# Kernel optimization log

Hardware: AMD Instinct MI355X
Metric: run time of the kernel (lower is better)

## Reference

```python
import jax, jax.numpy as jnp
import numpy as np

B, N, D, H = 2048, 64, 256, 16

def setup_inputs() -> dict:
    key = jax.random.key(0)
    ks = jax.random.split(key, 6)
    members_embeds = jax.random.normal(ks[0], (B, N, D), dtype=jnp.float32)
    item_embeds = jax.random.normal(ks[1], (B, D), dtype=jnp.float32)
    # MLP params: Linear(D,16) -> ReLU -> Linear(16,1)
    W1 = jax.random.normal(ks[2], (D, H), dtype=jnp.float32) * (1.0 / np.sqrt(D))
    b1 = jnp.zeros((H,), dtype=jnp.float32)
    W2 = jax.random.normal(ks[3], (H, 1), dtype=jnp.float32) * (1.0 / np.sqrt(H))
    b2 = jnp.zeros((1,), dtype=jnp.float32)
    return {"members_embeds": members_embeds, "item_embeds": item_embeds,
            "W1": W1, "b1": b1, "W2": W2, "b2": b2}

def reference(members_embeds, item_embeds, W1, b1, W2, b2):
    # Original: diff_i = sum_{j != i} (u_i - u_j) * item  ==  (N*u_i - sum_j u_j) * item
    n = members_embeds.shape[1]
    total = jnp.sum(members_embeds, axis=1, keepdims=True)           # [B,1,D]
    diff = (n * members_embeds - total) * item_embeds[:, None, :]    # [B,N,D]
    h = jax.nn.relu(jnp.einsum('bnd,dh->bnh', diff, W1) + b1)        # [B,N,16]
    logits = (jnp.einsum('bnh,ho->bno', h, W2) + b2)[..., 0]         # [B,N]
    return jax.nn.softmax(logits, axis=1)                            # weights over members
```

## Files before the change

### kernel.cpp

```cpp
#include <hip/hip_runtime.h>


static constexpr int NMEM  = 64;
static constexpr int DDIM  = 256;
static constexpr int TD    = 32;
static constexpr int NTILE = DDIM / TD;
static constexpr int UTS4  = TD / 4;

__device__ __forceinline__ void fma4(float4& acc, float s, const float4& w) {
    acc.x = fmaf(s, w.x, acc.x);
    acc.y = fmaf(s, w.y, acc.y);
    acc.z = fmaf(s, w.z, acc.z);
    acc.w = fmaf(s, w.w, acc.w);
}

__global__ __launch_bounds__(256, 2)
void attn_group_softmax(const float* __restrict__ u_g,
                        const float* __restrict__ item_g,
                        const float* __restrict__ W1,
                        const float* __restrict__ b1,
                        const float* __restrict__ W2,
                        float* __restrict__ out)
{
    __shared__ float w1s[DDIM * 16];
    __shared__ float ut[4][NMEM * TD];

    const int tid  = threadIdx.x;
    const int w    = tid >> 6;
    const int lane = tid & 63;
    const int b    = blockIdx.x * 4 + w;

    {
        const float4* src = (const float4*)W1;
        float4* dst = (float4*)w1s;
        #pragma unroll
        for (int i = 0; i < 4; ++i) dst[tid + 256 * i] = src[tid + 256 * i];
    }
    __syncthreads();

    const int q    = lane & 3;
    const int n0   = lane >> 2;
    const int col4 = lane & 7;
    const int row0 = lane >> 3;
    const int sc   = col4 ^ row0;
    const int pk   = n0 & 7;

    const float4* ug4  = (const float4*)u_g + (size_t)b * (NMEM * DDIM / 4);
    const float4* ig4  = (const float4*)(item_g + (size_t)b * DDIM);
    float4*       uts4 = (float4*)ut[w];
    const float4* utf4 = (const float4*)ut[w];
    const float4* w1s4 = (const float4*)w1s;

    float4 itv[NTILE];
    #pragma unroll
    for (int t = 0; t < NTILE; ++t) itv[t] = ig4[t * 8 + col4];

    float4 acc0 = make_float4(0.f, 0.f, 0.f, 0.f);
    float4 acc1 = acc0, acc2 = acc0, acc3 = acc0;

    float4 r[8];
    #pragma unroll
    for (int i = 0; i < 8; ++i)
        r[i] = ug4[(row0 + 8 * i) * (DDIM / 4) + col4];

    for (int t = 0; t < NTILE; ++t) {
        const float4 iv = itv[t];
        #pragma unroll
        for (int i = 0; i < 8; ++i) {
            float4 v = r[i];
            v.x *= iv.x; v.y *= iv.y; v.z *= iv.z; v.w *= iv.w;
            uts4[(row0 + 8 * i) * UTS4 + sc] = v;
        }
        if (t + 1 < NTILE) {
            #pragma unroll
            for (int i = 0; i < 8; ++i)
                r[i] = ug4[(row0 + 8 * i) * (DDIM / 4) + (t + 1) * 8 + col4];
        }

        #pragma unroll
        for (int d4 = 0; d4 < TD / 4; ++d4) {
            const int p = d4 ^ pk;
            const float4 ua = utf4[(n0     ) * UTS4 + p];
            const float4 ub = utf4[(n0 + 16) * UTS4 + p];
            const float4 uc = utf4[(n0 + 32) * UTS4 + p];
            const float4 ud = utf4[(n0 + 48) * UTS4 + p];
            const int dbase = (t * TD + d4 * 4) * 4 + q;
            const float4 w0  = w1s4[dbase];
            const float4 w1r = w1s4[dbase + 4];
            const float4 w2r = w1s4[dbase + 8];
            const float4 w3r = w1s4[dbase + 12];
            fma4(acc0, ua.x, w0); fma4(acc0, ua.y, w1r); fma4(acc0, ua.z, w2r); fma4(acc0, ua.w, w3r);
            fma4(acc1, ub.x, w0); fma4(acc1, ub.y, w1r); fma4(acc1, ub.z, w2r); fma4(acc1, ub.w, w3r);
            fma4(acc2, uc.x, w0); fma4(acc2, uc.y, w1r); fma4(acc2, uc.z, w2r); fma4(acc2, uc.w, w3r);
            fma4(acc3, ud.x, w0); fma4(acc3, ud.y, w1r); fma4(acc3, ud.z, w2r); fma4(acc3, ud.w, w3r);
        }
    }

    float4 tt;
    tt.x = acc0.x + acc1.x + acc2.x + acc3.x;
    tt.y = acc0.y + acc1.y + acc2.y + acc3.y;
    tt.z = acc0.z + acc1.z + acc2.z + acc3.z;
    tt.w = acc0.w + acc1.w + acc2.w + acc3.w;
    #pragma unroll
    for (int off = 4; off <= 32; off <<= 1) {
        tt.x += __shfl_xor(tt.x, off, 64);
        tt.y += __shfl_xor(tt.y, off, 64);
        tt.z += __shfl_xor(tt.z, off, 64);
        tt.w += __shfl_xor(tt.w, off, 64);
    }

    const float4 b1v = ((const float4*)b1)[q];
    const float4 w2v = ((const float4*)W2)[q];

    auto logit_part = [&](const float4& a) -> float {
        const float zx = fmaxf(fmaf(64.f, a.x, b1v.x - tt.x), 0.f);
        const float zy = fmaxf(fmaf(64.f, a.y, b1v.y - tt.y), 0.f);
        const float zz = fmaxf(fmaf(64.f, a.z, b1v.z - tt.z), 0.f);
        const float zw = fmaxf(fmaf(64.f, a.w, b1v.w - tt.w), 0.f);
        return zx * w2v.x + zy * w2v.y + zz * w2v.z + zw * w2v.w;
    };

    float p0 = logit_part(acc0);
    float p1 = logit_part(acc1);
    float p2 = logit_part(acc2);
    float p3 = logit_part(acc3);
    p0 += __shfl_xor(p0, 1, 64); p0 += __shfl_xor(p0, 2, 64);
    p1 += __shfl_xor(p1, 1, 64); p1 += __shfl_xor(p1, 2, 64);
    p2 += __shfl_xor(p2, 1, 64); p2 += __shfl_xor(p2, 2, 64);
    p3 += __shfl_xor(p3, 1, 64); p3 += __shfl_xor(p3, 2, 64);

    float m = fmaxf(fmaxf(p0, p1), fmaxf(p2, p3));
    #pragma unroll
    for (int off = 4; off <= 32; off <<= 1) m = fmaxf(m, __shfl_xor(m, off, 64));
    const float e0 = __expf(p0 - m);
    const float e1 = __expf(p1 - m);
    const float e2 = __expf(p2 - m);
    const float e3 = __expf(p3 - m);
    float s = e0 + e1 + e2 + e3;
    #pragma unroll
    for (int off = 4; off <= 32; off <<= 1) s += __shfl_xor(s, off, 64);
    const float inv = 1.0f / s;

    if (q == 0) {
        float* ob = out + (size_t)b * NMEM + n0;
        ob[0]  = e0 * inv;
        ob[16] = e1 * inv;
        ob[32] = e2 * inv;
        ob[48] = e3 * inv;
    }
}

extern "C" void kernel_launch(void* const* d_in, const int* in_sizes, int n_in,
                              void* d_out, int out_size, void* d_ws, size_t ws_size,
                              hipStream_t stream) {
    const float* u    = (const float*)d_in[0];
    const float* item = (const float*)d_in[1];
    const float* W1   = (const float*)d_in[2];
    const float* b1   = (const float*)d_in[3];
    const float* W2   = (const float*)d_in[4];
    (void)in_sizes; (void)n_in; (void)out_size; (void)d_ws; (void)ws_size;

    attn_group_softmax<<<512, 256, 0, stream>>>(u, item, W1, b1, W2, (float*)d_out);
}
```

Measured before the change: 209.3 us.

## Compute projection from registers with per-lane partial sums and shuffle reductions

```diff
diff --git a/kernel.cpp b/kernel.cpp
--- a/kernel.cpp
+++ b/kernel.cpp
@@ -3,15 +3,20 @@
 
 static constexpr int NMEM  = 64;
 static constexpr int DDIM  = 256;
-static constexpr int TD    = 32;
-static constexpr int NTILE = DDIM / TD;
-static constexpr int UTS4  = TD / 4;
+static constexpr int NTILE = 8;
 
-__device__ __forceinline__ void fma4(float4& acc, float s, const float4& w) {
-    acc.x = fmaf(s, w.x, acc.x);
-    acc.y = fmaf(s, w.y, acc.y);
-    acc.z = fmaf(s, w.z, acc.z);
-    acc.w = fmaf(s, w.w, acc.w);
+__device__ __forceinline__ void fma4(float4& a, float s, const float4& w) {
+    a.x = fmaf(s, w.x, a.x); a.y = fmaf(s, w.y, a.y);
+    a.z = fmaf(s, w.z, a.z); a.w = fmaf(s, w.w, a.w);
+}
+__device__ __forceinline__ float4 shfl4x(const float4& v, int m) {
+    float4 r;
+    r.x = __shfl_xor(v.x, m, 64); r.y = __shfl_xor(v.y, m, 64);
+    r.z = __shfl_xor(v.z, m, 64); r.w = __shfl_xor(v.w, m, 64);
+    return r;
+}
+__device__ __forceinline__ void add4(float4& a, const float4& b) {
+    a.x += b.x; a.y += b.y; a.z += b.z; a.w += b.w;
 }
 
 __global__ __launch_bounds__(256, 2)
@@ -22,132 +27,131 @@
                         const float* __restrict__ W2,
                         float* __restrict__ out)
 {
-    __shared__ float w1s[DDIM * 16];
-    __shared__ float ut[4][NMEM * TD];
-
     const int tid  = threadIdx.x;
     const int w    = tid >> 6;
     const int lane = tid & 63;
     const int b    = blockIdx.x * 4 + w;
+    const int row0 = lane >> 3;
+    const int col4 = lane & 7;
 
-    {
-        const float4* src = (const float4*)W1;
-        float4* dst = (float4*)w1s;
-        #pragma unroll
-        for (int i = 0; i < 4; ++i) dst[tid + 256 * i] = src[tid + 256 * i];
-    }
-    __syncthreads();
+    const float4* ug4 = (const float4*)u_g + (size_t)b * (NMEM * DDIM / 4);
+    const float4* ig4 = (const float4*)(item_g + (size_t)b * DDIM);
+    const float4* w14 = (const float4*)W1;
 
-    const int q    = lane & 3;
-    const int n0   = lane >> 2;
-    const int col4 = lane & 7;
-    const int row0 = lane >> 3;
-    const int sc   = col4 ^ row0;
-    const int pk   = n0 & 7;
-
-    const float4* ug4  = (const float4*)u_g + (size_t)b * (NMEM * DDIM / 4);
-    const float4* ig4  = (const float4*)(item_g + (size_t)b * DDIM);
-    float4*       uts4 = (float4*)ut[w];
-    const float4* utf4 = (const float4*)ut[w];
-    const float4* w1s4 = (const float4*)w1s;
-
-    float4 itv[NTILE];
-    #pragma unroll
-    for (int t = 0; t < NTILE; ++t) itv[t] = ig4[t * 8 + col4];
-
-    float4 acc0 = make_float4(0.f, 0.f, 0.f, 0.f);
-    float4 acc1 = acc0, acc2 = acc0, acc3 = acc0;
-
-    float4 r[8];
+    float4 acc[8][4];
     #pragma unroll
     for (int i = 0; i < 8; ++i)
-        r[i] = ug4[(row0 + 8 * i) * (DDIM / 4) + col4];
+        #pragma unroll
+        for (int g = 0; g < 4; ++g)
+            acc[i][g] = make_float4(0.f, 0.f, 0.f, 0.f);
 
+    float4 uc[8], un[8];
+    #pragma unroll
+    for (int i = 0; i < 8; ++i)
+        uc[i] = ug4[(row0 + 8 * i) * (DDIM / 4) + col4];
+    float4 itc = ig4[col4];
+    float4 itn = itc;
+
+    #pragma unroll
     for (int t = 0; t < NTILE; ++t) {
-        const float4 iv = itv[t];
+        if (t + 1 < NTILE) {
+            #pragma unroll
+            for (int i = 0; i < 8; ++i)
+                un[i] = ug4[(row0 + 8 * i) * (DDIM / 4) + (t + 1) * 8 + col4];
+            itn = ig4[(t + 1) * 8 + col4];
+        }
+        const int rbase = (col4 + 8 * t) * 4;
         #pragma unroll
-        for (int i = 0; i < 8; ++i) {
-            float4 v = r[i];
-            v.x *= iv.x; v.y *= iv.y; v.z *= iv.z; v.w *= iv.w;
-            uts4[(row0 + 8 * i) * UTS4 + sc] = v;
+        for (int j = 0; j < 4; ++j) {
+            const float4 wr0 = w14[(rbase + j) * 4 + 0];
+            const float4 wr1 = w14[(rbase + j) * 4 + 1];
+            const float4 wr2 = w14[(rbase + j) * 4 + 2];
+            const float4 wr3 = w14[(rbase + j) * 4 + 3];
+            const float itj = (j == 0) ? itc.x : (j == 1) ? itc.y
+                            : (j == 2) ? itc.z : itc.w;
+            #pragma unroll
+            for (int i = 0; i < 8; ++i) {
+                const float uj = (j == 0) ? uc[i].x : (j == 1) ? uc[i].y
+                               : (j == 2) ? uc[i].z : uc[i].w;
+                const float s = uj * itj;
+                fma4(acc[i][0], s, wr0);
+                fma4(acc[i][1], s, wr1);
+                fma4(acc[i][2], s, wr2);
+                fma4(acc[i][3], s, wr3);
+            }
         }
         if (t + 1 < NTILE) {
             #pragma unroll
-            for (int i = 0; i < 8; ++i)
-                r[i] = ug4[(row0 + 8 * i) * (DDIM / 4) + (t + 1) * 8 + col4];
-        }
-
-        #pragma unroll
-        for (int d4 = 0; d4 < TD / 4; ++d4) {
-            const int p = d4 ^ pk;
-            const float4 ua = utf4[(n0     ) * UTS4 + p];
-            const float4 ub = utf4[(n0 + 16) * UTS4 + p];
-            const float4 uc = utf4[(n0 + 32) * UTS4 + p];
-            const float4 ud = utf4[(n0 + 48) * UTS4 + p];
-            const int dbase = (t * TD + d4 * 4) * 4 + q;
-            const float4 w0  = w1s4[dbase];
-            const float4 w1r = w1s4[dbase + 4];
-            const float4 w2r = w1s4[dbase + 8];
-            const float4 w3r = w1s4[dbase + 12];
-            fma4(acc0, ua.x, w0); fma4(acc0, ua.y, w1r); fma4(acc0, ua.z, w2r); fma4(acc0, ua.w, w3r);
-            fma4(acc1, ub.x, w0); fma4(acc1, ub.y, w1r); fma4(acc1, ub.z, w2r); fma4(acc1, ub.w, w3r);
-            fma4(acc2, uc.x, w0); fma4(acc2, uc.y, w1r); fma4(acc2, uc.z, w2r); fma4(acc2, uc.w, w3r);
-            fma4(acc3, ud.x, w0); fma4(acc3, ud.y, w1r); fma4(acc3, ud.z, w2r); fma4(acc3, ud.w, w3r);
+            for (int i = 0; i < 8; ++i) uc[i] = un[i];
+            itc = itn;
         }
     }
 
-    float4 tt;
-    tt.x = acc0.x + acc1.x + acc2.x + acc3.x;
-    tt.y = acc0.y + acc1.y + acc2.y + acc3.y;
-    tt.z = acc0.z + acc1.z + acc2.z + acc3.z;
-    tt.w = acc0.w + acc1.w + acc2.w + acc3.w;
     #pragma unroll
-    for (int off = 4; off <= 32; off <<= 1) {
-        tt.x += __shfl_xor(tt.x, off, 64);
-        tt.y += __shfl_xor(tt.y, off, 64);
-        tt.z += __shfl_xor(tt.z, off, 64);
-        tt.w += __shfl_xor(tt.w, off, 64);
+    for (int m = 1; m <= 4; m <<= 1)
+        #pragma unroll
+        for (int i = 0; i < 8; ++i)
+            #pragma unroll
+            for (int g = 0; g < 4; ++g)
+                add4(acc[i][g], shfl4x(acc[i][g], m));
+
+    float4 tt[4];
+    #pragma unroll
+    for (int g = 0; g < 4; ++g) {
+        tt[g] = acc[0][g];
+        #pragma unroll
+        for (int i = 1; i < 8; ++i) add4(tt[g], acc[i][g]);
+        #pragma unroll
+        for (int m = 8; m <= 32; m <<= 1) add4(tt[g], shfl4x(tt[g], m));
     }
 
-    const float4 b1v = ((const float4*)b1)[q];
-    const float4 w2v = ((const float4*)W2)[q];
+    const float4* b14 = (const float4*)b1;
+    const float4* w24 = (const float4*)W2;
+    float4 bt[4], w2v[4];
+    #pragma unroll
+    for (int g = 0; g < 4; ++g) {
+        const float4 bb = b14[g];
+        bt[g]  = make_float4(bb.x - tt[g].x, bb.y - tt[g].y,
+                             bb.z - tt[g].z, bb.w - tt[g].w);
+        w2v[g] = w24[g];
+    }
 
-    auto logit_part = [&](const float4& a) -> float {
-        const float zx = fmaxf(fmaf(64.f, a.x, b1v.x - tt.x), 0.f);
-        const float zy = fmaxf(fmaf(64.f, a.y, b1v.y - tt.y), 0.f);
-        const float zz = fmaxf(fmaf(64.f, a.z, b1v.z - tt.z), 0.f);
-        const float zw = fmaxf(fmaf(64.f, a.w, b1v.w - tt.w), 0.f);
-        return zx * w2v.x + zy * w2v.y + zz * w2v.z + zw * w2v.w;
-    };
+    float lp[8];
+    #pragma unroll
+    for (int i = 0; i < 8; ++i) {
+        float p = 0.f;
+        #pragma unroll
+        for (int g = 0; g < 4; ++g) {
+            const float zx = fmaxf(fmaf(64.f, acc[i][g].x, bt[g].x), 0.f);
+            const float zy = fmaxf(fmaf(64.f, acc[i][g].y, bt[g].y), 0.f);
+            const float zz = fmaxf(fmaf(64.f, acc[i][g].z, bt[g].z), 0.f);
+            const float zw = fmaxf(fmaf(64.f, acc[i][g].w, bt[g].w), 0.f);
+            p += zx * w2v[g].x + zy * w2v[g].y + zz * w2v[g].z + zw * w2v[g].w;
+        }
+        lp[i] = p;
+    }
 
-    float p0 = logit_part(acc0);
-    float p1 = logit_part(acc1);
-    float p2 = logit_part(acc2);
-    float p3 = logit_part(acc3);
-    p0 += __shfl_xor(p0, 1, 64); p0 += __shfl_xor(p0, 2, 64);
-    p1 += __shfl_xor(p1, 1, 64); p1 += __shfl_xor(p1, 2, 64);
-    p2 += __shfl_xor(p2, 1, 64); p2 += __shfl_xor(p2, 2, 64);
-    p3 += __shfl_xor(p3, 1, 64); p3 += __shfl_xor(p3, 2, 64);
-
-    float m = fmaxf(fmaxf(p0, p1), fmaxf(p2, p3));
+    float mx = lp[0];
     #pragma unroll
-    for (int off = 4; off <= 32; off <<= 1) m = fmaxf(m, __shfl_xor(m, off, 64));
-    const float e0 = __expf(p0 - m);
-    const float e1 = __expf(p1 - m);
-    const float e2 = __expf(p2 - m);
-    const float e3 = __expf(p3 - m);
-    float s = e0 + e1 + e2 + e3;
+    for (int i = 1; i < 8; ++i) mx = fmaxf(mx, lp[i]);
     #pragma unroll
-    for (int off = 4; off <= 32; off <<= 1) s += __shfl_xor(s, off, 64);
+    for (int m = 8; m <= 32; m <<= 1) mx = fmaxf(mx, __shfl_xor(mx, m, 64));
+    float e[8], s = 0.f;
+    #pragma unroll
+    for (int i = 0; i < 8; ++i) { e[i] = __expf(lp[i] - mx); s += e[i]; }
+    #pragma unroll
+    for (int m = 8; m <= 32; m <<= 1) s += __shfl_xor(s, m, 64);
     const float inv = 1.0f / s;
 
-    if (q == 0) {
-        float* ob = out + (size_t)b * NMEM + n0;
-        ob[0]  = e0 * inv;
-        ob[16] = e1 * inv;
-        ob[32] = e2 * inv;
-        ob[48] = e3 * inv;
-    }
+    float ev = e[0];
+    ev = (col4 == 1) ? e[1] : ev;
+    ev = (col4 == 2) ? e[2] : ev;
+    ev = (col4 == 3) ? e[3] : ev;
+    ev = (col4 == 4) ? e[4] : ev;
+    ev = (col4 == 5) ? e[5] : ev;
+    ev = (col4 == 6) ? e[6] : ev;
+    ev = (col4 == 7) ? e[7] : ev;
+    out[(size_t)b * NMEM + row0 + 8 * col4] = ev * inv;
 }
 
 extern "C" void kernel_launch(void* const* d_in, const int* in_sizes, int n_in,
```

After: 264.4 us. +26.3%, slower.

## Stream member tiles straight into LDS with double-buffered async global_load_lds

Applied to the files above, without the earlier changes.

```diff
diff --git a/kernel.cpp b/kernel.cpp
--- a/kernel.cpp
+++ b/kernel.cpp
@@ -1,17 +1,16 @@
 #include <hip/hip_runtime.h>
 
 
-static constexpr int NMEM  = 64;
-static constexpr int DDIM  = 256;
-static constexpr int TD    = 32;
-static constexpr int NTILE = DDIM / TD;
-static constexpr int UTS4  = TD / 4;
+static constexpr int NMEM = 64;
+static constexpr int DDIM = 256;
+static constexpr int NTILE = 8;
 
-__device__ __forceinline__ void fma4(float4& acc, float s, const float4& w) {
-    acc.x = fmaf(s, w.x, acc.x);
-    acc.y = fmaf(s, w.y, acc.y);
-    acc.z = fmaf(s, w.z, acc.z);
-    acc.w = fmaf(s, w.w, acc.w);
+__device__ __forceinline__ void fma4(float4& a, float s, const float4& w) {
+    a.x = fmaf(s, w.x, a.x); a.y = fmaf(s, w.y, a.y);
+    a.z = fmaf(s, w.z, a.z); a.w = fmaf(s, w.w, a.w);
+}
+__device__ __forceinline__ float rdlane(float v, int srclane) {
+    return __int_as_float(__builtin_amdgcn_readlane(__float_as_int(v), srclane));
 }
 
 __global__ __launch_bounds__(256, 2)
@@ -23,7 +22,7 @@
                         float* __restrict__ out)
 {
     __shared__ float w1s[DDIM * 16];
-    __shared__ float ut[4][NMEM * TD];
+    __shared__ float tiles[4][2][NMEM * 32];
 
     const int tid  = threadIdx.x;
     const int w    = tid >> 6;
@@ -36,65 +35,79 @@
         #pragma unroll
         for (int i = 0; i < 4; ++i) dst[tid + 256 * i] = src[tid + 256 * i];
     }
+    const float4 it4 = ((const float4*)(item_g + (size_t)b * DDIM))[lane];
     __syncthreads();
 
     const int q    = lane & 3;
     const int n0   = lane >> 2;
-    const int col4 = lane & 7;
-    const int row0 = lane >> 3;
-    const int sc   = col4 ^ row0;
     const int pk   = n0 & 7;
+    const int sco  = (lane & 7) ^ (lane >> 3);
 
-    const float4* ug4  = (const float4*)u_g + (size_t)b * (NMEM * DDIM / 4);
-    const float4* ig4  = (const float4*)(item_g + (size_t)b * DDIM);
-    float4*       uts4 = (float4*)ut[w];
-    const float4* utf4 = (const float4*)ut[w];
+    const float4* gstage = (const float4*)u_g + (size_t)b * (NMEM * DDIM / 4)
+                         + (lane >> 3) * (DDIM / 4) + sco;
+    float* const tb0 = &tiles[w][0][0];
+    float* const tb1 = &tiles[w][1][0];
     const float4* w1s4 = (const float4*)w1s;
 
-    float4 itv[NTILE];
-    #pragma unroll
-    for (int t = 0; t < NTILE; ++t) itv[t] = ig4[t * 8 + col4];
+    auto stage = [&](int t, float* lb) {
+        const float4* g = gstage + t * 8;
+        #pragma unroll
+        for (int k = 0; k < 8; ++k)
+            __builtin_amdgcn_global_load_lds(
+                (const __attribute__((address_space(1))) void*)(g + k * 512),
+                (__attribute__((address_space(3))) void*)(lb + k * 256),
+                16, 0, 0);
+    };
 
     float4 acc0 = make_float4(0.f, 0.f, 0.f, 0.f);
     float4 acc1 = acc0, acc2 = acc0, acc3 = acc0;
 
-    float4 r[8];
-    #pragma unroll
-    for (int i = 0; i < 8; ++i)
-        r[i] = ug4[(row0 + 8 * i) * (DDIM / 4) + col4];
+    auto compute_tile = [&](int t, const float* lb) {
+        const float4* lb4 = (const float4*)lb;
+        #pragma unroll
+        for (int d4 = 0; d4 < 8; ++d4) {
+            const int f = t * 8 + d4;
+            const float itx = rdlane(it4.x, f);
+            const float ity = rdlane(it4.y, f);
+            const float itz = rdlane(it4.z, f);
+            const float itw = rdlane(it4.w, f);
+            const int p = d4 ^ pk;
+            const float4 ua = lb4[(n0     ) * 8 + p];
+            const float4 ub = lb4[(n0 + 16) * 8 + p];
+            const float4 uc = lb4[(n0 + 32) * 8 + p];
+            const float4 ud = lb4[(n0 + 48) * 8 + p];
+            const int wb = (t * 32 + d4 * 4) * 4 + q;
+            const float4 w0  = w1s4[wb];
+            const float4 w1r = w1s4[wb + 4];
+            const float4 w2r = w1s4[wb + 8];
+            const float4 w3r = w1s4[wb + 12];
+            {   const float s0 = ua.x*itx, s1 = ua.y*ity, s2 = ua.z*itz, s3 = ua.w*itw;
+                fma4(acc0, s0, w0); fma4(acc0, s1, w1r);
+                fma4(acc0, s2, w2r); fma4(acc0, s3, w3r); }
+            {   const float s0 = ub.x*itx, s1 = ub.y*ity, s2 = ub.z*itz, s3 = ub.w*itw;
+                fma4(acc1, s0, w0); fma4(acc1, s1, w1r);
+                fma4(acc1, s2, w2r); fma4(acc1, s3, w3r); }
+            {   const float s0 = uc.x*itx, s1 = uc.y*ity, s2 = uc.z*itz, s3 = uc.w*itw;
+                fma4(acc2, s0, w0); fma4(acc2, s1, w1r);
+                fma4(acc2, s2, w2r); fma4(acc2, s3, w3r); }
+            {   const float s0 = ud.x*itx, s1 = ud.y*ity, s2 = ud.z*itz, s3 = ud.w*itw;
+                fma4(acc3, s0, w0); fma4(acc3, s1, w1r);
+                fma4(acc3, s2, w2r); fma4(acc3, s3, w3r); }
+        }
+    };
 
-    for (int t = 0; t < NTILE; ++t) {
-        const float4 iv = itv[t];
-        #pragma unroll
-        for (int i = 0; i < 8; ++i) {
-            float4 v = r[i];
-            v.x *= iv.x; v.y *= iv.y; v.z *= iv.z; v.w *= iv.w;
-            uts4[(row0 + 8 * i) * UTS4 + sc] = v;
-        }
-        if (t + 1 < NTILE) {
-            #pragma unroll
-            for (int i = 0; i < 8; ++i)
-                r[i] = ug4[(row0 + 8 * i) * (DDIM / 4) + (t + 1) * 8 + col4];
-        }
-
-        #pragma unroll
-        for (int d4 = 0; d4 < TD / 4; ++d4) {
-            const int p = d4 ^ pk;
-            const float4 ua = utf4[(n0     ) * UTS4 + p];
-            const float4 ub = utf4[(n0 + 16) * UTS4 + p];
-            const float4 uc = utf4[(n0 + 32) * UTS4 + p];
-            const float4 ud = utf4[(n0 + 48) * UTS4 + p];
-            const int dbase = (t * TD + d4 * 4) * 4 + q;
-            const float4 w0  = w1s4[dbase];
-            const float4 w1r = w1s4[dbase + 4];
-            const float4 w2r = w1s4[dbase + 8];
-            const float4 w3r = w1s4[dbase + 12];
-            fma4(acc0, ua.x, w0); fma4(acc0, ua.y, w1r); fma4(acc0, ua.z, w2r); fma4(acc0, ua.w, w3r);
-            fma4(acc1, ub.x, w0); fma4(acc1, ub.y, w1r); fma4(acc1, ub.z, w2r); fma4(acc1, ub.w, w3r);
-            fma4(acc2, uc.x, w0); fma4(acc2, uc.y, w1r); fma4(acc2, uc.z, w2r); fma4(acc2, uc.w, w3r);
-            fma4(acc3, ud.x, w0); fma4(acc3, ud.y, w1r); fma4(acc3, ud.z, w2r); fma4(acc3, ud.w, w3r);
-        }
+    stage(0, tb0);
+    stage(1, tb1);
+    #pragma unroll 1
+    for (int t = 0; t < 7; ++t) {
+        asm volatile("s_waitcnt vmcnt(8)" ::: "memory");
+        float* lb = (t & 1) ? tb1 : tb0;
+        compute_tile(t, lb);
+        asm volatile("s_waitcnt lgkmcnt(0)" ::: "memory");
+        if (t < 6) stage(t + 2, lb);
     }
+    asm volatile("s_waitcnt vmcnt(0)" ::: "memory");
+    compute_tile(7, tb1);
 
     float4 tt;
     tt.x = acc0.x + acc1.x + acc2.x + acc3.x;
```

Result: slower. 235.9 us (+12.7%).
